# Performance work log

Measured on AMD Instinct MI355X. Metric: run time of the kernel, lower is better.

The kernel has to match this reference:

```python
import jax, jax.numpy as jnp
import numpy as np

# hypers
R_CUT = 5.0      # 'cutoff radius'
N_MAX = 8        # radial channels
L_MAX = 3        # max spherical-harmonic degree
N_ATOMS = 20000
N_PAIRS = 500000
N_SPECIES = 4    # len(all_species)
N_PSEUDO = 2     # 'alchemical'


def setup_inputs() -> dict:
    key = jax.random.key(0)
    k1, k2, k3, k4, k5 = jax.random.split(key, 5)
    positions = jax.random.normal(k1, (N_ATOMS, 3), dtype=jnp.float32) * 2.0
    centers = jax.random.randint(k2, (N_PAIRS,), 0, N_ATOMS)
    neighbors = jax.random.randint(k3, (N_PAIRS,), 0, N_ATOMS)
    species_idx = jax.random.randint(k4, (N_ATOMS,), 0, N_SPECIES).astype(jnp.int32)
    W_comb = jax.random.normal(k5, (N_PSEUDO, N_SPECIES), dtype=jnp.float32)
    return {"positions": positions, "W_comb": W_comb, "centers": centers,
            "neighbors": neighbors, "species_idx": species_idx}


def _real_spherical_harmonics(x, y, z):
    """Real spherical harmonics Y_lm on unit vectors, l = 0..3.
    Returns list of arrays, each [P, 2l+1] ordered m = -l..l."""
    x2, y2, z2 = x * x, y * y, z * z
    Y0 = jnp.full_like(x, 0.28209479177387814)[:, None]
    c1 = 0.4886025119029199
    Y1 = jnp.stack([c1 * y, c1 * z, c1 * x], axis=-1)
    Y2 = jnp.stack([
        1.0925484305920792 * x * y,
        1.0925484305920792 * y * z,
        0.31539156525252005 * (3.0 * z2 - 1.0),
        1.0925484305920792 * x * z,
        0.5462742152960396 * (x2 - y2),
    ], axis=-1)
    Y3 = jnp.stack([
        0.5900435899266435 * y * (3.0 * x2 - y2),
        2.890611442640554 * x * y * z,
        0.4570457994644658 * y * (5.0 * z2 - 1.0),
        0.3731763325901154 * z * (5.0 * z2 - 3.0),
        0.4570457994644658 * x * (5.0 * z2 - 1.0),
        1.445305721320277 * z * (x2 - y2),
        0.5900435899266435 * x * (x2 - 3.0 * y2),
    ], axis=-1)
    return [Y0, Y1, Y2, Y3]


def reference(positions, W_comb, centers, neighbors, species_idx):
    # pairwise displacement vectors (gather over neighbor list)
    vec = positions[neighbors] - positions[centers]            # [P, 3]
    r = jnp.sqrt((vec * vec).sum(-1) + 1e-12)                  # [P]
    u = vec / r[:, None]                                       # unit vectors

    # smooth radial basis with cosine cutoff (Gaussians on a grid)
    fc = jnp.where(r < R_CUT, 0.5 * (jnp.cos(jnp.pi * r / R_CUT) + 1.0), 0.0)
    cn = jnp.linspace(0.0, R_CUT, N_MAX, dtype=positions.dtype)
    sigma = R_CUT / N_MAX
    radial = jnp.exp(-0.5 * ((r[:, None] - cn) / sigma) ** 2) * fc[:, None]  # [P, n]

    # alchemical combination: one_hot(species_neighbor) @ W_comb.T -> [P, q]
    w = W_comb.T[species_idx[neighbors]]                       # [P, q]
    feat = w[:, :, None] * radial[:, None, :]                  # [P, q, n]

    sph = _real_spherical_harmonics(u[:, 0], u[:, 1], u[:, 2])

    blocks = []
    for Yl in sph:
        # per-pair outer product: [P, 2l+1, q, n]
        exp_l = Yl[:, :, None, None] * feat[:, None, :, :]
        # sum over neighbors j for each center i (scatter-add)
        summed = jax.ops.segment_sum(exp_l, centers, num_segments=N_ATOMS)
        blocks.append(summed.reshape(N_ATOMS, Yl.shape[1], N_PSEUDO * N_MAX))
    # concatenate all l blocks along the component (m) axis: [N_atoms, 16, q*n]
    return jnp.concatenate(blocks, axis=1)
```

## Files before the change

### kernel.cpp

```cpp
#include <hip/hip_runtime.h>
#include <math.h>

#define N_SPECIES 4
#define NMAX      8
#define RCUT      5.0f
#define CAP       64


__global__ void zero_kernel(int* __restrict__ cnt, int n) {
    int i = blockIdx.x * blockDim.x + threadIdx.x;
    if (i < n) cnt[i] = 0;
}

__global__ void build_kernel(const int* __restrict__ centers,
                             const int* __restrict__ neighbors,
                             const int* __restrict__ species,
                             int* __restrict__ cnt,
                             int* __restrict__ bin, int P) {
    int p = blockIdx.x * blockDim.x + threadIdx.x;
    if (p < P) {
        int c = centers[p];
        int j = neighbors[p];
        int s = species[j];
        int idx = atomicAdd(&cnt[c], 1);
        if (idx < CAP) bin[c * CAP + idx] = j | (s << 16);
    }
}


__global__ __launch_bounds__(256) void accum_kernel(
        const float* __restrict__ pos,
        const float* __restrict__ W,
        const int*  __restrict__ cnt,
        const int*  __restrict__ bin,
        float* __restrict__ out, int N) {
    const int wave = threadIdx.x >> 6;
    const int lane = threadIdx.x & 63;
    const int i = blockIdx.x * 4 + wave;

    __shared__ __align__(16) float sY[4][64][20];
    __shared__ __align__(16) float sF[4][64][20];

    int ci = 0;
    if (i < N) { ci = cnt[i]; if (ci > CAP) ci = CAP; }

    if (lane < ci) {
        const float pix = pos[3 * i], piy = pos[3 * i + 1], piz = pos[3 * i + 2];
        int payload = bin[i * CAP + lane];
        int j = payload & 0xFFFF;
        int s = payload >> 16;

        float dx = pos[3 * j]     - pix;
        float dy = pos[3 * j + 1] - piy;
        float dz = pos[3 * j + 2] - piz;
        float r  = sqrtf(dx * dx + dy * dy + dz * dz + 1e-12f);
        float inv = 1.0f / r;
        float x = dx * inv, y = dy * inv, z = dz * inv;

        float fc = (r < RCUT) ? 0.5f * (cosf(3.14159265358979323846f * (r / RCUT)) + 1.0f)
                              : 0.0f;

        const float Ck[NMAX] = {
            1.0f,          5.2045002e-1f, 7.3369700e-2f, 2.8016300e-3f,
            2.8977800e-5f, 8.1185700e-8f, 6.1609600e-11f, 1.2664166e-14f };
        float rc = (r < RCUT) ? r : RCUT;
        float A  = expf(-1.28f * r * r) * fc;
        float B  = expf(1.82857143f * rc);

        int w_s = s;
        float w0 = W[w_s];
        float w1 = W[N_SPECIES + w_s];

        float* Fr = sF[wave][lane];
        float pw = A;
        float f0[NMAX];
        #pragma unroll
        for (int k = 0; k < NMAX; ++k) {
            float radk = pw * Ck[k];
            f0[k] = radk;
            pw *= B;
        }
        ((float4*)Fr)[0] = make_float4(w0 * f0[0], w0 * f0[1], w0 * f0[2], w0 * f0[3]);
        ((float4*)Fr)[1] = make_float4(w0 * f0[4], w0 * f0[5], w0 * f0[6], w0 * f0[7]);
        ((float4*)Fr)[2] = make_float4(w1 * f0[0], w1 * f0[1], w1 * f0[2], w1 * f0[3]);
        ((float4*)Fr)[3] = make_float4(w1 * f0[4], w1 * f0[5], w1 * f0[6], w1 * f0[7]);

        float x2 = x * x, y2 = y * y, z2 = z * z;
        float* Yr = sY[wave][lane];
        ((float4*)Yr)[0] = make_float4(
            0.28209479177387814f,
            0.4886025119029199f * y,
            0.4886025119029199f * z,
            0.4886025119029199f * x);
        ((float4*)Yr)[1] = make_float4(
            1.0925484305920792f * x * y,
            1.0925484305920792f * y * z,
            0.31539156525252005f * (3.0f * z2 - 1.0f),
            1.0925484305920792f * x * z);
        ((float4*)Yr)[2] = make_float4(
            0.5462742152960396f * (x2 - y2),
            0.5900435899266435f * y * (3.0f * x2 - y2),
            2.890611442640554f  * x * y * z,
            0.4570457994644658f * y * (5.0f * z2 - 1.0f));
        ((float4*)Yr)[3] = make_float4(
            0.3731763325901154f * z * (5.0f * z2 - 3.0f),
            0.4570457994644658f * x * (5.0f * z2 - 1.0f),
            1.445305721320277f  * z * (x2 - y2),
            0.5900435899266435f * x * (x2 - 3.0f * y2));
    }
    __syncthreads();

    const int m  = lane >> 2;
    const int cg = lane & 3;
    float ax = 0.f, ay = 0.f, az = 0.f, aw = 0.f;
    #pragma unroll 4
    for (int l = 0; l < ci; ++l) {
        float yv = sY[wave][l][m];
        float4 f = *(const float4*)&sF[wave][l][cg * 4];
        ax = fmaf(yv, f.x, ax);
        ay = fmaf(yv, f.y, ay);
        az = fmaf(yv, f.z, az);
        aw = fmaf(yv, f.w, aw);
    }
    if (i < N) {
        float4 o = make_float4(ax, ay, az, aw);
        *(float4*)&out[(size_t)i * 256 + (size_t)lane * 4] = o;
    }
}


extern "C" void kernel_launch(void* const* d_in, const int* in_sizes, int n_in,
                              void* d_out, int out_size, void* d_ws, size_t ws_size,
                              hipStream_t stream) {
    const float* positions = (const float*)d_in[0];
    const float* W_comb    = (const float*)d_in[1];
    const int*   centers   = (const int*)d_in[2];
    const int*   neighbors = (const int*)d_in[3];
    const int*   species   = (const int*)d_in[4];
    float* out = (float*)d_out;

    const int P = in_sizes[2];
    const int N = in_sizes[4];

    int* cnt = (int*)d_ws;
    int* bin = cnt + N;

    zero_kernel<<<(N + 255) / 256, 256, 0, stream>>>(cnt, N);
    build_kernel<<<(P + 255) / 256, 256, 0, stream>>>(centers, neighbors, species,
                                                      cnt, bin, P);
    accum_kernel<<<(N + 3) / 4, 256, 0, stream>>>(positions, W_comb, cnt, bin,
                                                  out, N);
}
```

Measured before the change: 114.2 us.

## Pack positions with species, pad atomic counters, use one-wave blocks

Adds a prep kernel that packs each atom's position and species into a float4, so the accumulation kernel does one vector gather per neighbor and the build kernel no longer gathers species. Per-center counters are padded to 64-byte strides to cut atomic contention and false sharing, and they are zeroed with hipMemsetAsync. The accumulation kernel now launches one 64-thread block per atom and does the geometry math before the lane<ci check, so unused lanes read bin entries that were never written (their index is clamped to stay in range). The trade-offs are an extra kernel launch, a memset sixteen times larger than before, and more blocks to schedule.

```diff
diff --git a/kernel.cpp b/kernel.cpp
--- a/kernel.cpp
+++ b/kernel.cpp
@@ -4,89 +4,88 @@
 #define N_SPECIES 4
 #define NMAX      8
 #define RCUT      5.0f
-#define CAP       64
+#define CAP        64
+#define CNT_STRIDE 16
 
 
-__global__ void zero_kernel(int* __restrict__ cnt, int n) {
+__global__ void prep_kernel(const float* __restrict__ pos,
+                            const int*  __restrict__ species,
+                            float4* __restrict__ posw, int N) {
     int i = blockIdx.x * blockDim.x + threadIdx.x;
-    if (i < n) cnt[i] = 0;
+    if (i < N) {
+        posw[i] = make_float4(pos[3 * i], pos[3 * i + 1], pos[3 * i + 2],
+                              __int_as_float(species[i]));
+    }
 }
+
 
 __global__ void build_kernel(const int* __restrict__ centers,
                              const int* __restrict__ neighbors,
-                             const int* __restrict__ species,
                              int* __restrict__ cnt,
                              int* __restrict__ bin, int P) {
     int p = blockIdx.x * blockDim.x + threadIdx.x;
     if (p < P) {
         int c = centers[p];
         int j = neighbors[p];
-        int s = species[j];
-        int idx = atomicAdd(&cnt[c], 1);
-        if (idx < CAP) bin[c * CAP + idx] = j | (s << 16);
+        int idx = atomicAdd(&cnt[c * CNT_STRIDE], 1);
+        if (idx < CAP) bin[c * CAP + idx] = j;
     }
 }
 
 
-__global__ __launch_bounds__(256) void accum_kernel(
-        const float* __restrict__ pos,
-        const float* __restrict__ W,
-        const int*  __restrict__ cnt,
-        const int*  __restrict__ bin,
+__global__ __launch_bounds__(64) void accum_kernel(
+        const float4* __restrict__ posw,
+        const float*  __restrict__ W,
+        const int*    __restrict__ cnt,
+        const int*    __restrict__ bin,
         float* __restrict__ out, int N) {
-    const int wave = threadIdx.x >> 6;
-    const int lane = threadIdx.x & 63;
-    const int i = blockIdx.x * 4 + wave;
+    const int i    = blockIdx.x;
+    const int lane = threadIdx.x;
 
-    __shared__ __align__(16) float sY[4][64][20];
-    __shared__ __align__(16) float sF[4][64][20];
+    __shared__ __align__(16) float sY[64][20];
+    __shared__ __align__(16) float sF[64][20];
 
-    int ci = 0;
-    if (i < N) { ci = cnt[i]; if (ci > CAP) ci = CAP; }
+    int payload = bin[i * CAP + lane];
+    int ci = cnt[i * CNT_STRIDE];
+    if (ci > CAP) ci = CAP;
+    int j = payload;
+    if ((unsigned)j >= (unsigned)N) j = 0;
+    float4 pj = posw[j];
+    float4 pi = posw[i];
+
+    float dx = pj.x - pi.x, dy = pj.y - pi.y, dz = pj.z - pi.z;
+    float r  = sqrtf(dx * dx + dy * dy + dz * dz + 1e-12f);
+    float inv = 1.0f / r;
+    float x = dx * inv, y = dy * inv, z = dz * inv;
+
+    float fc = (r < RCUT) ? 0.5f * (cosf(3.14159265358979323846f * (r / RCUT)) + 1.0f)
+                          : 0.0f;
+
+    const float Ck[NMAX] = {
+        1.0f,          5.2045002e-1f, 7.3369700e-2f, 2.8016300e-3f,
+        2.8977800e-5f, 8.1185700e-8f, 6.1609600e-11f, 1.2664166e-14f };
+    float rc = (r < RCUT) ? r : RCUT;
+    float A  = expf(-1.28f * r * r) * fc;
+    float B  = expf(1.82857143f * rc);
+
+    int s = __float_as_int(pj.w);
+    float w0 = W[s];
+    float w1 = W[N_SPECIES + s];
+
+    float f0[NMAX];
+    float pw = A;
+    #pragma unroll
+    for (int k = 0; k < NMAX; ++k) { f0[k] = pw * Ck[k]; pw *= B; }
 
     if (lane < ci) {
-        const float pix = pos[3 * i], piy = pos[3 * i + 1], piz = pos[3 * i + 2];
-        int payload = bin[i * CAP + lane];
-        int j = payload & 0xFFFF;
-        int s = payload >> 16;
-
-        float dx = pos[3 * j]     - pix;
-        float dy = pos[3 * j + 1] - piy;
-        float dz = pos[3 * j + 2] - piz;
-        float r  = sqrtf(dx * dx + dy * dy + dz * dz + 1e-12f);
-        float inv = 1.0f / r;
-        float x = dx * inv, y = dy * inv, z = dz * inv;
-
-        float fc = (r < RCUT) ? 0.5f * (cosf(3.14159265358979323846f * (r / RCUT)) + 1.0f)
-                              : 0.0f;
-
-        const float Ck[NMAX] = {
-            1.0f,          5.2045002e-1f, 7.3369700e-2f, 2.8016300e-3f,
-            2.8977800e-5f, 8.1185700e-8f, 6.1609600e-11f, 1.2664166e-14f };
-        float rc = (r < RCUT) ? r : RCUT;
-        float A  = expf(-1.28f * r * r) * fc;
-        float B  = expf(1.82857143f * rc);
-
-        int w_s = s;
-        float w0 = W[w_s];
-        float w1 = W[N_SPECIES + w_s];
-
-        float* Fr = sF[wave][lane];
-        float pw = A;
-        float f0[NMAX];
-        #pragma unroll
-        for (int k = 0; k < NMAX; ++k) {
-            float radk = pw * Ck[k];
-            f0[k] = radk;
-            pw *= B;
-        }
+        float* Fr = sF[lane];
         ((float4*)Fr)[0] = make_float4(w0 * f0[0], w0 * f0[1], w0 * f0[2], w0 * f0[3]);
         ((float4*)Fr)[1] = make_float4(w0 * f0[4], w0 * f0[5], w0 * f0[6], w0 * f0[7]);
         ((float4*)Fr)[2] = make_float4(w1 * f0[0], w1 * f0[1], w1 * f0[2], w1 * f0[3]);
         ((float4*)Fr)[3] = make_float4(w1 * f0[4], w1 * f0[5], w1 * f0[6], w1 * f0[7]);
 
         float x2 = x * x, y2 = y * y, z2 = z * z;
-        float* Yr = sY[wave][lane];
+        float* Yr = sY[lane];
         ((float4*)Yr)[0] = make_float4(
             0.28209479177387814f,
             0.4886025119029199f * y,
@@ -115,17 +114,15 @@
     float ax = 0.f, ay = 0.f, az = 0.f, aw = 0.f;
     #pragma unroll 4
     for (int l = 0; l < ci; ++l) {
-        float yv = sY[wave][l][m];
-        float4 f = *(const float4*)&sF[wave][l][cg * 4];
+        float yv = sY[l][m];
+        float4 f = *(const float4*)&sF[l][cg * 4];
         ax = fmaf(yv, f.x, ax);
         ay = fmaf(yv, f.y, ay);
         az = fmaf(yv, f.z, az);
         aw = fmaf(yv, f.w, aw);
     }
-    if (i < N) {
-        float4 o = make_float4(ax, ay, az, aw);
-        *(float4*)&out[(size_t)i * 256 + (size_t)lane * 4] = o;
-    }
+    float4 o = make_float4(ax, ay, az, aw);
+    *(float4*)&out[(size_t)i * 256 + (size_t)lane * 4] = o;
 }
 
 
@@ -142,12 +139,12 @@
     const int P = in_sizes[2];
     const int N = in_sizes[4];
 
-    int* cnt = (int*)d_ws;
-    int* bin = cnt + N;
+    float4* posw = (float4*)d_ws;
+    int*    cnt  = (int*)(posw + N);
+    int*    bin  = cnt + (size_t)N * CNT_STRIDE;
 
-    zero_kernel<<<(N + 255) / 256, 256, 0, stream>>>(cnt, N);
-    build_kernel<<<(P + 255) / 256, 256, 0, stream>>>(centers, neighbors, species,
-                                                      cnt, bin, P);
-    accum_kernel<<<(N + 3) / 4, 256, 0, stream>>>(positions, W_comb, cnt, bin,
-                                                  out, N);
+    hipMemsetAsync(cnt, 0, (size_t)N * CNT_STRIDE * sizeof(int), stream);
+    prep_kernel<<<(N + 255) / 256, 256, 0, stream>>>(positions, species, posw, N);
+    build_kernel<<<(P + 255) / 256, 256, 0, stream>>>(centers, neighbors, cnt, bin, P);
+    accum_kernel<<<N, 64, 0, stream>>>(posw, W_comb, cnt, bin, out, N);
 }
```

After: 110.9 us. -2.9%, faster.
